# Kernel tuning notes

Hardware: AMD Instinct MI355X
Metric: run time of the kernel (lower is better)

Reference implementation:

```python
import jax, jax.numpy as jnp
import numpy as np
from jax import lax

N_EXPERTS = 16
TOP_K = 2
D_MODEL = 512
D_FF = 2048


def setup_inputs() -> dict:
    key = jax.random.key(0)
    ks = jax.random.split(key, 7)
    s_in = 1.0 / np.sqrt(D_MODEL)
    s_ff = 1.0 / np.sqrt(D_FF)
    x = jax.random.normal(ks[0], (2, 2048, D_MODEL), dtype=jnp.float32)
    router_w = jax.random.uniform(ks[1], (N_EXPERTS, D_MODEL), jnp.float32, -s_in, s_in)
    router_b = jax.random.uniform(ks[2], (N_EXPERTS,), jnp.float32, -s_in, s_in)
    w1 = jax.random.uniform(ks[3], (N_EXPERTS, D_FF, D_MODEL), jnp.float32, -s_in, s_in)
    b1 = jax.random.uniform(ks[4], (N_EXPERTS, D_FF), jnp.float32, -s_in, s_in)
    w2 = jax.random.uniform(ks[5], (N_EXPERTS, D_MODEL, D_FF), jnp.float32, -s_ff, s_ff)
    b2 = jax.random.uniform(ks[6], (N_EXPERTS, D_MODEL), jnp.float32, -s_ff, s_ff)
    return {"x": x, "router_w": router_w, "router_b": router_b,
            "w1": w1, "b1": b1, "w2": w2, "b2": b2}


def reference(x, router_w, router_b, w1, b1, w2, b2):
    B, S, D = x.shape
    xt = x.reshape(-1, D)                                   # [T, D]
    logits = xt @ router_w.T + router_b                     # [T, E]
    probs = jax.nn.softmax(logits, axis=-1)
    topk_p, topk_i = lax.top_k(probs, TOP_K)                # [T, K]
    # Dense gate matrix: gate[t, e] = topk prob if expert e selected else 0.
    # Weighting by gate reproduces the masked gather/scatter-add exactly.
    onehot = jax.nn.one_hot(topk_i, N_EXPERTS, dtype=probs.dtype)  # [T, K, E]
    gates = jnp.sum(onehot * topk_p[..., None], axis=1)     # [T, E]

    def expert_step(acc, packed):
        w1e, b1e, w2e, b2e, ge = packed                     # per-expert params + gate col [T]
        h = jax.nn.gelu(xt @ w1e.T + b1e, approximate=False)  # [T, D_FF]
        y = h @ w2e.T + b2e                                 # [T, D]
        return acc + y * ge[:, None], None

    out, _ = lax.scan(expert_step, jnp.zeros_like(xt),
                      (w1, b1, w2, b2, gates.T))
    return out.reshape(B, S, D)
```

## Files before the change

kernel.cpp:

```cpp
#include <hip/hip_runtime.h>
#include <stdint.h>

#define T_TOK 4096
#define DM    512
#define DFF   2048
#define NE    16
#define NSLOT (T_TOK * 2)
#define NW    (16 * 2048 * 512)
#define MAXTILE 80
#define CONVB 4096
#define ROUTB (T_TOK / 4)
#define KSPLIT 2

typedef __attribute__((ext_vector_type(8))) short  bf16x8;
typedef __attribute__((ext_vector_type(4))) float  f32x4;
typedef __attribute__((ext_vector_type(8))) unsigned short us8;

static __device__ __forceinline__ unsigned short f2bf(float f) {
    unsigned int u = __float_as_uint(f);
    u += 0x7FFFu + ((u >> 16) & 1u);
    return (unsigned short)(u >> 16);
}

static __device__ __forceinline__ void gload_lds16(const void* g, void* l) {
    __builtin_amdgcn_global_load_lds(
        (const __attribute__((address_space(1))) void*)g,
        (__attribute__((address_space(3))) void*)l, 16, 0, 0);
}

static __device__ __forceinline__ int xcd_chunk_logical(int bid, int total) {
    int k = bid & 7, seq = bid >> 3;
    int q = total >> 3, r = total & 7;
    int base = k * q + (k < r ? k : r);
    int len  = q + (k < r ? 1 : 0);
    return (seq < len) ? (base + seq) : total;
}

__global__ __launch_bounds__(256) void convert_router_kernel(
    const float* __restrict__ w1, const float* __restrict__ w2,
    unsigned short* __restrict__ w1b, unsigned short* __restrict__ w2b,
    const float* __restrict__ x, const float* __restrict__ rw,
    const float* __restrict__ rb, int* __restrict__ tok_e,
    float* __restrict__ tok_g, unsigned short* __restrict__ xb)
{
    __shared__ float rws[NE * DM];
    int tid = threadIdx.x;

    if (blockIdx.x >= ROUTB) {
        size_t base = (size_t)(blockIdx.x - ROUTB) * 8192;
        const float* src; unsigned short* dst;
        if (base < (size_t)NW) { src = w1 + base;        dst = w1b + base; }
        else                   { src = w2 + (base - NW); dst = w2b + (base - NW); }
#pragma unroll
        for (int it = 0; it < 4; ++it) {
            int off2 = it * 2048 + tid * 8;
            f32x4 a = __builtin_nontemporal_load((const f32x4*)(src + off2));
            f32x4 b = __builtin_nontemporal_load((const f32x4*)(src + off2 + 4));
            us8 v;
            v[0] = f2bf(a.x); v[1] = f2bf(a.y); v[2] = f2bf(a.z); v[3] = f2bf(a.w);
            v[4] = f2bf(b.x); v[5] = f2bf(b.y); v[6] = f2bf(b.z); v[7] = f2bf(b.w);
            *(us8*)(dst + off2) = v;
        }
        return;
    }

    for (int i = 0; i < 8; ++i) {
        int idx = (tid + i * 256) * 4;
        *(f32x4*)&rws[idx] = *(const f32x4*)&rw[idx];
    }
    __syncthreads();

    int wid = tid >> 6, lane = tid & 63;
    int t = blockIdx.x * 4 + wid;

    float xv[8];
    const float* xp = x + (size_t)t * DM + lane * 8;
    *(f32x4*)&xv[0] = *(const f32x4*)xp;
    *(f32x4*)&xv[4] = *(const f32x4*)(xp + 4);

    us8 v;
    for (int i = 0; i < 8; ++i) v[i] = f2bf(xv[i]);
    *(us8*)&xb[(size_t)t * DM + lane * 8] = v;

    float acc[NE];
    for (int e = 0; e < NE; ++e) {
        const float* wp = &rws[e * DM + lane * 8];
        float a = 0.f;
        for (int i = 0; i < 8; ++i) a += xv[i] * wp[i];
        acc[e] = a;
    }
    for (int e = 0; e < NE; ++e) {
        float v2 = acc[e];
        for (int off = 32; off > 0; off >>= 1) v2 += __shfl_xor(v2, off);
        acc[e] = v2 + rb[e];
    }
    float m = acc[0];
    for (int e = 1; e < NE; ++e) m = fmaxf(m, acc[e]);
    float p[NE]; float s = 0.f;
    for (int e = 0; e < NE; ++e) { p[e] = expf(acc[e] - m); s += p[e]; }
    float inv = 1.f / s;
    int i0 = 0; float p0 = p[0];
    for (int e = 1; e < NE; ++e) if (p[e] > p0) { p0 = p[e]; i0 = e; }
    int i1 = (i0 == 0) ? 1 : 0; float p1 = p[i1];
    for (int e = 0; e < NE; ++e)
        if (e != i0 && p[e] > p1) { p1 = p[e]; i1 = e; }
    if (lane == 0) {
        tok_e[t * 2]     = i0;  tok_e[t * 2 + 1] = i1;
        tok_g[t * 2]     = p0 * inv;
        tok_g[t * 2 + 1] = p1 * inv;
    }
}

__global__ __launch_bounds__(1024) void compact_kernel(
    const int* __restrict__ tok_e, int* __restrict__ slot_token,
    int* __restrict__ tok_slot, int* __restrict__ eoff)
{
    __shared__ int wsum[16][NE];
    __shared__ int wbase[16][NE];
    __shared__ int ebl[NE];
    int tid = threadIdx.x;
    int wv = tid >> 6, lane = tid & 63;

    int ent[8];
    *(int4*)&ent[0] = *(const int4*)&tok_e[tid * 8];
    *(int4*)&ent[4] = *(const int4*)&tok_e[tid * 8 + 4];

    int cnt[NE], isc[NE];
#pragma unroll
    for (int e = 0; e < NE; ++e) {
        int c = 0;
#pragma unroll
        for (int i = 0; i < 8; ++i) c += (ent[i] == e) ? 1 : 0;
        int v = c;
#pragma unroll
        for (int off = 1; off < 64; off <<= 1) {
            int u = __shfl_up(v, off);
            if (lane >= off) v += u;
        }
        cnt[e] = c; isc[e] = v;
    }
    if (lane == 63) {
#pragma unroll
        for (int e = 0; e < NE; ++e) wsum[wv][e] = isc[e];
    }
    __syncthreads();
    if (wv == 0 && lane < NE) {
        int e = lane, s = 0;
#pragma unroll
        for (int w = 0; w < 16; ++w) { wbase[w][e] = s; s += wsum[w][e]; }
        int til = (s + 127) >> 7;
        int rs = s, rt = til;
#pragma unroll
        for (int off = 1; off < 16; off <<= 1) {
            int u1 = __shfl_up(rs, off);
            int u2 = __shfl_up(rt, off);
            if (lane >= off) { rs += u1; rt += u2; }
        }
        ebl[e] = rs - s;
        eoff[e] = rs - s;
        eoff[16 + e] = s;
        eoff[32 + e] = rt - til;
        if (e == NE - 1) eoff[48] = rt;
    }
    __syncthreads();
    int ofs[NE];
#pragma unroll
    for (int e = 0; e < NE; ++e)
        ofs[e] = ebl[e] + wbase[wv][e] + isc[e] - cnt[e];
#pragma unroll
    for (int i = 0; i < 8; ++i) {
        int ei = ent[i], s = 0;
#pragma unroll
        for (int e = 0; e < NE; ++e) if (ei == e) s = ofs[e];
        slot_token[s] = tid * 4 + (i >> 1);
        tok_slot[tid * 8 + i] = s;
#pragma unroll
        for (int e = 0; e < NE; ++e) if (ei == e) ofs[e] = s + 1;
    }
}

__global__ __launch_bounds__(256) void gemm1_kernel(
    const unsigned short* __restrict__ xb, const unsigned short* __restrict__ w1b,
    const float* __restrict__ b1, const int* __restrict__ slot_token,
    const int* __restrict__ eoff, unsigned short* __restrict__ h)
{
    __shared__ unsigned short smem[32768];
    __shared__ int tokrow[128];
    __shared__ int meta[49];

    int tid = threadIdx.x;
    if (tid < 49) meta[tid] = eoff[tid];
    __syncthreads();

    int lg = xcd_chunk_logical(blockIdx.x, meta[48] * 16);
    int slot_idx = lg >> 4;
    if (slot_idx >= meta[48]) return;
    int nB = (lg & 15) * 128;
    int e = 0;
    while (e < NE - 1 && meta[32 + e + 1] <= slot_idx) ++e;
    int mt  = slot_idx - meta[32 + e];
    int off = meta[e], cnt = meta[16 + e];
    int slot0 = off + mt * 128;
    int valid = cnt - mt * 128; if (valid > 128) valid = 128;

    if (tid < 128) {
        int s = slot0 + tid; if (s > NSLOT - 1) s = NSLOT - 1;
        tokrow[tid] = slot_token[s];
    }
    __syncthreads();

    f32x4 acc[16];
    for (int i = 0; i < 16; ++i) acc[i] = (f32x4){0.f, 0.f, 0.f, 0.f};

    const unsigned short* wb = w1b + ((size_t)e * DFF + nB) * DM;
    int wid = tid >> 6, l = tid & 63;
    int wm = (wid & 1) * 64, wn = (wid >> 1) * 64;
    int q = l >> 4, c = l & 15;

    auto stage = [&](int buf, int kt) {
        unsigned short* A = &smem[buf * 16384];
        unsigned short* B = A + 8192;
        for (int j = 0; j < 4; ++j) {
            int u = (wid * 4 + j) * 64 + l;
            int row = u >> 3, sc = (u & 7) ^ (row & 7);
            gload_lds16(xb + (size_t)tokrow[row] * DM + kt * 64 + sc * 8, &A[u * 8]);
        }
        for (int j = 0; j < 4; ++j) {
            int u = (wid * 4 + j) * 64 + l;
            int row = u >> 3, sc = (u & 7) ^ (row & 7);
            gload_lds16(wb + (size_t)row * DM + kt * 64 + sc * 8, &B[u * 8]);
        }
    };

    stage(0, 0);
    __syncthreads();
    int cur = 0;
    for (int kt = 0; kt < DM / 64; ++kt) {
        if (kt + 1 < DM / 64) stage(cur ^ 1, kt + 1);
        unsigned short* A = &smem[cur * 16384];
        unsigned short* B = A + 8192;
        for (int ks = 0; ks < 2; ++ks) {
            int sw = ((ks * 4 + q) ^ (c & 7)) * 8;
            bf16x8 af[4], bv[4];
            for (int i = 0; i < 4; ++i) af[i] = *(bf16x8*)&A[(wm + i * 16 + c) * 64 + sw];
            for (int j = 0; j < 4; ++j) bv[j] = *(bf16x8*)&B[(wn + j * 16 + c) * 64 + sw];
            for (int i = 0; i < 4; ++i)
                for (int j = 0; j < 4; ++j)
                    acc[i * 4 + j] = __builtin_amdgcn_mfma_f32_16x16x32_bf16(
                        af[i], bv[j], acc[i * 4 + j], 0, 0, 0);
        }
        __syncthreads();
        cur ^= 1;
    }

    float bias[4];
    for (int j = 0; j < 4; ++j) bias[j] = b1[e * DFF + nB + wn + j * 16 + c];
    unsigned short* bounce = smem;
    for (int ph = 0; ph < 2; ++ph) {
        __syncthreads();
        for (int jj = 0; jj < 2; ++jj) {
            int j = 2 * ph + jj;
            for (int i = 0; i < 4; ++i) {
                f32x4 a = acc[i * 4 + j];
                for (int r = 0; r < 4; ++r) {
                    int rl = wm + i * 16 + q * 4 + r;
                    float z = a[r] + bias[j];
                    float u2 = z * fmaf(0.0356774081f, z * z, 0.7978845608f);
                    float ex = __expf(2.0f * u2);
                    float th = 1.0f - 2.0f * __builtin_amdgcn_rcpf(ex + 1.0f);
                    float g = 0.5f * z * (1.0f + th);
                    bounce[rl * 80 + (wn >> 1) + jj * 16 + c] = f2bf(g);
                }
            }
        }
        __syncthreads();
        for (int it = 0; it < 4; ++it) {
            int u2 = it * 256 + tid;
            int row = u2 >> 3, ch = u2 & 7;
            int cl = ch * 8;
            int n  = (cl < 32 ? cl : 32 + cl) + 32 * ph;
            if (row < valid)
                *(us8*)&h[(size_t)(slot0 + row) * DFF + nB + n] =
                    *(us8*)&bounce[row * 80 + cl];
        }
    }
}

__global__ __launch_bounds__(256) void gemm2_kernel(
    const unsigned short* __restrict__ h, const unsigned short* __restrict__ w2b,
    const int* __restrict__ eoff, float* __restrict__ y)
{
    __shared__ unsigned short smem[32768];
    __shared__ int meta[49];

    int tid = threadIdx.x;
    if (tid < 49) meta[tid] = eoff[tid];
    __syncthreads();

    int lg = xcd_chunk_logical(blockIdx.x, meta[48] * 8);
    int slot_idx = lg >> 3;
    if (slot_idx >= meta[48]) return;
    int nB = (lg & 3) * 128;
    int z  = (lg >> 2) & 1;
    int e = 0;
    while (e < NE - 1 && meta[32 + e + 1] <= slot_idx) ++e;
    int mt  = slot_idx - meta[32 + e];
    int off = meta[e], cnt = meta[16 + e];
    int slot0 = off + mt * 128;
    int valid = cnt - mt * 128; if (valid > 128) valid = 128;

    f32x4 acc[16];
    for (int i = 0; i < 16; ++i) acc[i] = (f32x4){0.f, 0.f, 0.f, 0.f};

    const unsigned short* wb = w2b + ((size_t)e * DM + nB) * DFF
                             + (size_t)z * (DFF / KSPLIT);
    const unsigned short* hz = h + (size_t)z * (DFF / KSPLIT);
    int wid = tid >> 6, l = tid & 63;
    int wm = (wid & 1) * 64, wn = (wid >> 1) * 64;
    int q = l >> 4, c = l & 15;

    auto stage = [&](int buf, int kt) {
        unsigned short* A = &smem[buf * 16384];
        unsigned short* B = A + 8192;
        for (int j = 0; j < 4; ++j) {
            int u = (wid * 4 + j) * 64 + l;
            int row = u >> 3, sc = (u & 7) ^ (row & 7);
            size_t s = slot0 + row; if (s > NSLOT - 1) s = NSLOT - 1;
            gload_lds16(hz + s * DFF + kt * 64 + sc * 8, &A[u * 8]);
        }
        for (int j = 0; j < 4; ++j) {
            int u = (wid * 4 + j) * 64 + l;
            int row = u >> 3, sc = (u & 7) ^ (row & 7);
            gload_lds16(wb + (size_t)row * DFF + kt * 64 + sc * 8, &B[u * 8]);
        }
    };

    const int NT = DFF / (64 * KSPLIT);
    stage(0, 0);
    __syncthreads();
    int cur = 0;
    for (int kt = 0; kt < NT; ++kt) {
        if (kt + 1 < NT) stage(cur ^ 1, kt + 1);
        unsigned short* A = &smem[cur * 16384];
        unsigned short* B = A + 8192;
        for (int ks = 0; ks < 2; ++ks) {
            int sw = ((ks * 4 + q) ^ (c & 7)) * 8;
            bf16x8 af[4], bv[4];
            for (int i = 0; i < 4; ++i) af[i] = *(bf16x8*)&A[(wm + i * 16 + c) * 64 + sw];
            for (int j = 0; j < 4; ++j) bv[j] = *(bf16x8*)&B[(wn + j * 16 + c) * 64 + sw];
            for (int i = 0; i < 4; ++i)
                for (int j = 0; j < 4; ++j)
                    acc[i * 4 + j] = __builtin_amdgcn_mfma_f32_16x16x32_bf16(
                        af[i], bv[j], acc[i * 4 + j], 0, 0, 0);
        }
        __syncthreads();
        cur ^= 1;
    }

    float* yz = y + (size_t)z * NSLOT * DM;
    for (int i = 0; i < 4; ++i)
        for (int j = 0; j < 4; ++j) {
            int n = nB + wn + j * 16 + c;
            for (int r = 0; r < 4; ++r) {
                int rl = wm + i * 16 + q * 4 + r;
                if (rl < valid)
                    yz[(size_t)(slot0 + rl) * DM + n] = acc[i * 4 + j][r];
            }
        }
}

__global__ __launch_bounds__(256) void combine_kernel(
    const float* __restrict__ y, const float* __restrict__ b2,
    const int* __restrict__ tok_slot, const float* __restrict__ tok_g,
    const int* __restrict__ tok_e, float* __restrict__ out)
{
    int tid = threadIdx.x;
    int t = blockIdx.x * 2 + (tid >> 7);
    int d = (tid & 127) * 4;
    int s0 = tok_slot[t * 2], s1 = tok_slot[t * 2 + 1];
    float g0 = tok_g[t * 2], g1 = tok_g[t * 2 + 1];
    int e0 = tok_e[t * 2], e1 = tok_e[t * 2 + 1];
    const float* yB = y + (size_t)NSLOT * DM;
    f32x4 y0a = *(const f32x4*)&y [(size_t)s0 * DM + d];
    f32x4 y0b = *(const f32x4*)&yB[(size_t)s0 * DM + d];
    f32x4 y1a = *(const f32x4*)&y [(size_t)s1 * DM + d];
    f32x4 y1b = *(const f32x4*)&yB[(size_t)s1 * DM + d];
    f32x4 c0 = *(const f32x4*)&b2[e0 * DM + d];
    f32x4 c1 = *(const f32x4*)&b2[e1 * DM + d];
    f32x4 o;
    for (int i = 0; i < 4; ++i)
        o[i] = g0 * (y0a[i] + y0b[i] + c0[i]) + g1 * (y1a[i] + y1b[i] + c1[i]);
    *(f32x4*)&out[(size_t)t * DM + d] = o;
}

extern "C" void kernel_launch(void* const* d_in, const int* in_sizes, int n_in,
                              void* d_out, int out_size, void* d_ws, size_t ws_size,
                              hipStream_t stream) {
    const float* x  = (const float*)d_in[0];
    const float* rw = (const float*)d_in[1];
    const float* rb = (const float*)d_in[2];
    const float* w1 = (const float*)d_in[3];
    const float* b1 = (const float*)d_in[4];
    const float* w2 = (const float*)d_in[5];
    const float* b2 = (const float*)d_in[6];
    float* out = (float*)d_out;

    char* ws = (char*)d_ws;
    size_t o = 0;
    unsigned short* h   = (unsigned short*)(ws + o); o += (size_t)NSLOT * DFF * 2;
    unsigned short* w1b = (unsigned short*)(ws + o); o += (size_t)NW * 2;
    unsigned short* w2b = (unsigned short*)(ws + o); o += (size_t)NW * 2;
    unsigned short* xb  = (unsigned short*)(ws + o); o += (size_t)T_TOK * DM * 2;
    int*   tok_e      = (int*)(ws + o);   o += (size_t)NSLOT * 4;
    float* tok_g      = (float*)(ws + o); o += (size_t)NSLOT * 4;
    int*   tok_slot   = (int*)(ws + o);   o += (size_t)NSLOT * 4;
    int*   slot_token = (int*)(ws + o);   o += (size_t)NSLOT * 4;
    int*   eoff       = (int*)(ws + o);
    float* y = (float*)w1b;

    convert_router_kernel<<<ROUTB + CONVB, 256, 0, stream>>>(
        w1, w2, w1b, w2b, x, rw, rb, tok_e, tok_g, xb);
    compact_kernel<<<1, 1024, 0, stream>>>(
        tok_e, slot_token, tok_slot, eoff);
    gemm1_kernel<<<16 * MAXTILE, 256, 0, stream>>>(
        xb, w1b, b1, slot_token, eoff, h);
    gemm2_kernel<<<8 * MAXTILE, 256, 0, stream>>>(
        h, w2b, eoff, y);
    combine_kernel<<<T_TOK / 2, 256, 0, stream>>>(
        y, b2, tok_slot, tok_g, tok_e, out);
}
```

Baseline: 267.3 us.

## Fuse expert compaction into router kernel via last-block atomic counter

Removes the separate single-block compact kernel launch by having the last router block, detected through a global atomic counter and threadfences, perform the expert histogram, prefix sum and slot assignment with 256 threads handling 32 entries each. This saves a kernel launch and its dependency gap, but adds a memset, serializes compaction onto one 256-thread block, and relies on router blocks finishing before the conversion work. It also pads the GELU bounce buffer row stride from 80 to 88 elements to reduce LDS bank conflicts.

Result: slower. 334.7 us (+25.2%).

```diff
diff --git a/kernel.cpp b/kernel.cpp
--- a/kernel.cpp
+++ b/kernel.cpp
@@ -41,9 +41,15 @@
     unsigned short* __restrict__ w1b, unsigned short* __restrict__ w2b,
     const float* __restrict__ x, const float* __restrict__ rw,
     const float* __restrict__ rb, int* __restrict__ tok_e,
-    float* __restrict__ tok_g, unsigned short* __restrict__ xb)
+    float* __restrict__ tok_g, unsigned short* __restrict__ xb,
+    int* __restrict__ slot_token, int* __restrict__ tok_slot,
+    int* __restrict__ eoff, unsigned int* __restrict__ ctr)
 {
     __shared__ float rws[NE * DM];
+    __shared__ int wsum[4][NE];
+    __shared__ int wbase[4][NE];
+    __shared__ int ebl[NE];
+    __shared__ int lastf;
     int tid = threadIdx.x;
 
     if (blockIdx.x >= ROUTB) {
@@ -109,56 +115,52 @@
         tok_g[t * 2]     = p0 * inv;
         tok_g[t * 2 + 1] = p1 * inv;
     }
-}
-
-__global__ __launch_bounds__(1024) void compact_kernel(
-    const int* __restrict__ tok_e, int* __restrict__ slot_token,
-    int* __restrict__ tok_slot, int* __restrict__ eoff)
-{
-    __shared__ int wsum[16][NE];
-    __shared__ int wbase[16][NE];
-    __shared__ int ebl[NE];
-    int tid = threadIdx.x;
-    int wv = tid >> 6, lane = tid & 63;
-
-    int ent[8];
-    *(int4*)&ent[0] = *(const int4*)&tok_e[tid * 8];
-    *(int4*)&ent[4] = *(const int4*)&tok_e[tid * 8 + 4];
+
+    __threadfence();
+    if (tid == 0) lastf = (atomicAdd(ctr, 1u) == ROUTB - 1) ? 1 : 0;
+    __syncthreads();
+    if (!lastf) return;
+    __threadfence();
+
+    int ent[32];
+#pragma unroll
+    for (int i = 0; i < 8; ++i)
+        *(int4*)&ent[i * 4] = *(const int4*)&tok_e[tid * 32 + i * 4];
 
     int cnt[NE], isc[NE];
 #pragma unroll
     for (int e = 0; e < NE; ++e) {
-        int c = 0;
-#pragma unroll
-        for (int i = 0; i < 8; ++i) c += (ent[i] == e) ? 1 : 0;
-        int v = c;
+        int c2 = 0;
+#pragma unroll
+        for (int i = 0; i < 32; ++i) c2 += (ent[i] == e) ? 1 : 0;
+        int v2 = c2;
 #pragma unroll
         for (int off = 1; off < 64; off <<= 1) {
-            int u = __shfl_up(v, off);
-            if (lane >= off) v += u;
-        }
-        cnt[e] = c; isc[e] = v;
+            int u = __shfl_up(v2, off);
+            if (lane >= off) v2 += u;
+        }
+        cnt[e] = c2; isc[e] = v2;
     }
     if (lane == 63) {
 #pragma unroll
-        for (int e = 0; e < NE; ++e) wsum[wv][e] = isc[e];
-    }
-    __syncthreads();
-    if (wv == 0 && lane < NE) {
-        int e = lane, s = 0;
-#pragma unroll
-        for (int w = 0; w < 16; ++w) { wbase[w][e] = s; s += wsum[w][e]; }
-        int til = (s + 127) >> 7;
-        int rs = s, rt = til;
+        for (int e = 0; e < NE; ++e) wsum[wid][e] = isc[e];
+    }
+    __syncthreads();
+    if (wid == 0 && lane < NE) {
+        int e = lane, s2 = 0;
+#pragma unroll
+        for (int w = 0; w < 4; ++w) { wbase[w][e] = s2; s2 += wsum[w][e]; }
+        int til = (s2 + 127) >> 7;
+        int rs = s2, rt = til;
 #pragma unroll
         for (int off = 1; off < 16; off <<= 1) {
             int u1 = __shfl_up(rs, off);
             int u2 = __shfl_up(rt, off);
             if (lane >= off) { rs += u1; rt += u2; }
         }
-        ebl[e] = rs - s;
-        eoff[e] = rs - s;
-        eoff[16 + e] = s;
+        ebl[e] = rs - s2;
+        eoff[e] = rs - s2;
+        eoff[16 + e] = s2;
         eoff[32 + e] = rt - til;
         if (e == NE - 1) eoff[48] = rt;
     }
@@ -166,16 +168,16 @@
     int ofs[NE];
 #pragma unroll
     for (int e = 0; e < NE; ++e)
-        ofs[e] = ebl[e] + wbase[wv][e] + isc[e] - cnt[e];
-#pragma unroll
-    for (int i = 0; i < 8; ++i) {
-        int ei = ent[i], s = 0;
-#pragma unroll
-        for (int e = 0; e < NE; ++e) if (ei == e) s = ofs[e];
-        slot_token[s] = tid * 4 + (i >> 1);
-        tok_slot[tid * 8 + i] = s;
-#pragma unroll
-        for (int e = 0; e < NE; ++e) if (ei == e) ofs[e] = s + 1;
+        ofs[e] = ebl[e] + wbase[wid][e] + isc[e] - cnt[e];
+#pragma unroll
+    for (int i = 0; i < 32; ++i) {
+        int ei = ent[i], s2 = 0;
+#pragma unroll
+        for (int e = 0; e < NE; ++e) if (ei == e) s2 = ofs[e];
+        slot_token[s2] = tid * 16 + (i >> 1);
+        tok_slot[tid * 32 + i] = s2;
+#pragma unroll
+        for (int e = 0; e < NE; ++e) if (ei == e) ofs[e] = s2 + 1;
     }
 }
 
@@ -269,7 +271,7 @@
                     float ex = __expf(2.0f * u2);
                     float th = 1.0f - 2.0f * __builtin_amdgcn_rcpf(ex + 1.0f);
                     float g = 0.5f * z * (1.0f + th);
-                    bounce[rl * 80 + (wn >> 1) + jj * 16 + c] = f2bf(g);
+                    bounce[rl * 88 + (wn >> 1) + jj * 16 + c] = f2bf(g);
                 }
             }
         }
@@ -281,7 +283,7 @@
             int n  = (cl < 32 ? cl : 32 + cl) + 32 * ph;
             if (row < valid)
                 *(us8*)&h[(size_t)(slot0 + row) * DFF + nB + n] =
-                    *(us8*)&bounce[row * 80 + cl];
+                    *(us8*)&bounce[row * 88 + cl];
         }
     }
 }
@@ -415,13 +417,14 @@
     float* tok_g      = (float*)(ws + o); o += (size_t)NSLOT * 4;
     int*   tok_slot   = (int*)(ws + o);   o += (size_t)NSLOT * 4;
     int*   slot_token = (int*)(ws + o);   o += (size_t)NSLOT * 4;
-    int*   eoff       = (int*)(ws + o);
+    int*   eoff       = (int*)(ws + o);   o += 64 * 4;
+    unsigned int* ctr = (unsigned int*)(ws + o);
     float* y = (float*)w1b;
 
+    hipMemsetAsync(ctr, 0, 4, stream);
     convert_router_kernel<<<ROUTB + CONVB, 256, 0, stream>>>(
-        w1, w2, w1b, w2b, x, rw, rb, tok_e, tok_g, xb);
-    compact_kernel<<<1, 1024, 0, stream>>>(
-        tok_e, slot_token, tok_slot, eoff);
+        w1, w2, w1b, w2b, x, rw, rb, tok_e, tok_g, xb,
+        slot_token, tok_slot, eoff, ctr);
     gemm1_kernel<<<16 * MAXTILE, 256, 0, stream>>>(
         xb, w1b, b1, slot_token, eoff, h);
     gemm2_kernel<<<8 * MAXTILE, 256, 0, stream>>>(
```
